# Kernel tuning notes

Measured on AMD Instinct MI355X. Metric: run time of the kernel, lower is better.

The kernel has to match this reference:

```python
import jax, jax.numpy as jnp
import numpy as np
import math

WH, WW = 7, 7          # window size
N = WH * WW            # tokens per window = 49
H = 12                 # num heads
C = 384                # dim
D = C // H             # head dim = 32
NW = 64                # num windows (56x56 map, 7x7 windows)
B = 32                 # image batch
BW = B * NW            # windowed batch = 2048


def _cpb_constants():
    # log-spaced continuous relative coords table, flattened to [(2*WH-1)*(2*WW-1), 2]
    rh = np.arange(-(WH - 1), WH, dtype=np.float32)
    rw = np.arange(-(WW - 1), WW, dtype=np.float32)
    t = np.stack(np.meshgrid(rh, rw, indexing='ij'), axis=-1)  # [13,13,2]
    t[..., 0] /= (WH - 1)
    t[..., 1] /= (WW - 1)
    t *= 8.0
    t = np.sign(t) * np.log2(np.abs(t) + 1.0) / np.log2(8.0)
    # relative position index [N*N]
    ch, cw = np.meshgrid(np.arange(WH), np.arange(WW), indexing='ij')
    cf = np.stack([ch.ravel(), cw.ravel()])            # [2, N]
    rel = cf[:, :, None] - cf[:, None, :]              # [2, N, N]
    rel = rel.transpose(1, 2, 0).astype(np.int64)      # [N, N, 2]
    rel[..., 0] += WH - 1
    rel[..., 1] += WW - 1
    rel[..., 0] *= 2 * WW - 1
    rpi = rel.sum(-1).reshape(-1)                      # [N*N]
    return jnp.asarray(t.reshape(-1, 2)), jnp.asarray(rpi)

_COORDS_TABLE, _RPI = _cpb_constants()


def setup_inputs() -> dict:
    key = jax.random.key(0)
    ks = jax.random.split(key, 8)
    x = jax.random.normal(ks[0], (BW, N, C), dtype=jnp.float32)
    # shifted-window style 0/-100 mask
    mask = jnp.where(jax.random.uniform(ks[1], (NW, N, N)) < 0.1, -100.0, 0.0).astype(jnp.float32)
    qkv_w = jax.random.normal(ks[2], (3 * C, C), dtype=jnp.float32) * 0.02
    q_bias = jnp.zeros((C,), dtype=jnp.float32)
    v_bias = jnp.zeros((C,), dtype=jnp.float32)
    logit_scale = jnp.full((H, 1, 1), math.log(10.0), dtype=jnp.float32)
    cpb_w1 = jax.random.normal(ks[3], (512, 2), dtype=jnp.float32) * 0.02
    cpb_b1 = jnp.zeros((512,), dtype=jnp.float32)
    cpb_w2 = jax.random.normal(ks[4], (H, 512), dtype=jnp.float32) * 0.02
    proj_w = jax.random.normal(ks[5], (C, C), dtype=jnp.float32) * 0.02
    proj_b = jnp.zeros((C,), dtype=jnp.float32)
    return {"x": x, "mask": mask, "qkv_w": qkv_w, "q_bias": q_bias, "v_bias": v_bias,
            "logit_scale": logit_scale, "cpb_w1": cpb_w1, "cpb_b1": cpb_b1,
            "cpb_w2": cpb_w2, "proj_w": proj_w, "proj_b": proj_b}


def reference(x, mask, qkv_w, q_bias, v_bias, logit_scale, cpb_w1, cpb_b1, cpb_w2, proj_w, proj_b):
    B_, n, c = x.shape
    # qkv projection; k has no bias (registered zeros buffer)
    qkv_bias = jnp.concatenate([q_bias, jnp.zeros_like(q_bias), v_bias])
    qkv = x @ qkv_w.T + qkv_bias                              # [B_, N, 3C]
    qkv = qkv.reshape(B_, n, 3, H, D).transpose(2, 0, 3, 1, 4)  # [3, B_, H, N, D]
    q, k, v = qkv[0], qkv[1], qkv[2]
    # cosine attention
    qn = q / jnp.clip(jnp.linalg.norm(q, axis=-1, keepdims=True), 1e-12)
    kn = k / jnp.clip(jnp.linalg.norm(k, axis=-1, keepdims=True), 1e-12)
    attn = jnp.einsum('bhnd,bhmd->bhnm', qn, kn)              # [B_, H, N, N]
    scale = jnp.exp(jnp.minimum(logit_scale, math.log(1.0 / 0.01)))  # [H,1,1]
    attn = attn * scale
    # continuous position bias MLP + gather
    hid = jax.nn.relu(_COORDS_TABLE @ cpb_w1.T + cpb_b1)      # [169, 512]
    bias_tab = hid @ cpb_w2.T                                  # [169, H]
    rpb = bias_tab[_RPI].reshape(n, n, H).transpose(2, 0, 1)  # [H, N, N]
    rpb = 16.0 * jax.nn.sigmoid(rpb)
    attn = attn + rpb[None]
    # shifted-window mask add
    nW = mask.shape[0]
    attn = attn.reshape(B_ // nW, nW, H, n, n) + mask[None, :, None]
    attn = jax.nn.softmax(attn.reshape(B_, H, n, n), axis=-1)
    out = jnp.einsum('bhnm,bhmd->bnhd', attn, v).reshape(B_, n, c)
    return out @ proj_w.T + proj_b
```

## Files before the change

### kernel.cpp

```cpp
#include <hip/hip_runtime.h>
#include <hip/hip_bf16.h>
#include <math.h>

#define NTOK 49
#define NH 12
#define HD 32
#define CDIM 384
#define NWIN 64
#define BWIN 2048

typedef __bf16 bf16x8 __attribute__((ext_vector_type(8)));
typedef __bf16 bf16x4 __attribute__((ext_vector_type(4)));
typedef float f32x4 __attribute__((ext_vector_type(4)));

__device__ __forceinline__ void gload_lds16(const void* g, void* l) {
    __builtin_amdgcn_global_load_lds((const __attribute__((address_space(1))) void*)g,
                                     (__attribute__((address_space(3))) void*)l, 16, 0, 0);
}

__global__ void cvt_f32_bf16(const float* __restrict__ src, __bf16* __restrict__ dst, int n8) {
    int i = blockIdx.x * blockDim.x + threadIdx.x;
    if (i >= n8) return;
    f32x4 a = *(const f32x4*)(src + (size_t)i * 8);
    f32x4 b = *(const f32x4*)(src + (size_t)i * 8 + 4);
    bf16x8 o;
#pragma unroll
    for (int e = 0; e < 4; ++e) { o[e] = (__bf16)a[e]; o[e + 4] = (__bf16)b[e]; }
    *(bf16x8*)(dst + (size_t)i * 8) = o;
}

__global__ void cpb_mlp_kernel(const float* __restrict__ w1, const float* __restrict__ b1,
                               const float* __restrict__ w2, float* __restrict__ bias_tab) {
    int t = blockIdx.x * blockDim.x + threadIdx.x;
    if (t >= 169 * NH) return;
    int r = t / NH, h = t - (t / NH) * NH;
    int i = r / 13, j = r - (r / 13) * 13;
    float a0 = (float)(i - 6) * (8.0f / 6.0f);
    float a1 = (float)(j - 6) * (8.0f / 6.0f);
    float c0 = copysignf(log2f(fabsf(a0) + 1.0f) * (1.0f / 3.0f), a0);
    float c1 = copysignf(log2f(fabsf(a1) + 1.0f) * (1.0f / 3.0f), a1);
    float sum = 0.f;
    for (int k = 0; k < 512; ++k) {
        float hid = c0 * w1[2 * k] + c1 * w1[2 * k + 1] + b1[k];
        hid = fmaxf(hid, 0.f);
        sum += hid * w2[h * 512 + k];
    }
    bias_tab[r * NH + h] = sum;
}

__global__ void rpbT_kernel(const float* __restrict__ bias_tab, float* __restrict__ rpbT) {
    int idx = blockIdx.x * blockDim.x + threadIdx.x;
    if (idx >= NH * NTOK * NTOK) return;
    int h = idx / (NTOK * NTOK);
    int rem = idx - h * (NTOK * NTOK);
    int kj = rem / NTOK, qi = rem - (rem / NTOK) * NTOK;
    int chi = qi / 7, cwi = qi - chi * 7;
    int chj = kj / 7, cwj = kj - chj * 7;
    int rpi = (chi - chj + 6) * 13 + (cwi - cwj + 6);
    float x = bias_tab[rpi * NH + h];
    rpbT[idx] = 16.f / (1.f + __expf(-x));
}

__global__ void maskT_kernel(const float* __restrict__ mask, float* __restrict__ maskT) {
    int idx = blockIdx.x * blockDim.x + threadIdx.x;
    if (idx >= NWIN * NTOK * NTOK) return;
    int w = idx / (NTOK * NTOK);
    int rem = idx - w * (NTOK * NTOK);
    int kj = rem / NTOK, qi = rem - (rem / NTOK) * NTOK;
    maskT[idx] = mask[(w * NTOK + qi) * NTOK + kj];
}

template <int MODE, int NBY>
__global__ __launch_bounds__(256) void gemm3(
    const __bf16* __restrict__ A, const __bf16* __restrict__ Bw,
    const float* __restrict__ qbias, const float* __restrict__ vbias,
    __bf16* __restrict__ qkvout,
    float* __restrict__ fout, const float* __restrict__ fbias)
{
    __shared__ __bf16 As[2][128 * 32];
    __shared__ __bf16 Bs[2][128 * 32];
    const int tid = threadIdx.x;
    const int chunk = (784 * NBY) >> 3;
    const int wg = (blockIdx.x & 7) * chunk + (blockIdx.x >> 3);
    const int gx = wg / NBY, gy = wg - (wg / NBY) * NBY;
    const int lane = tid & 63;
    const int wid = tid >> 6;
    const int wr = (wid >> 1) * 64;
    const int wc = (wid & 1) * 64;
    const int fr = lane & 15;
    const int fq = lane >> 4;

    f32x4 acc[4][4];
#pragma unroll
    for (int m = 0; m < 4; ++m)
#pragma unroll
        for (int n = 0; n < 4; ++n)
            acc[m][n] = (f32x4){0.f, 0.f, 0.f, 0.f};

    const int srow0 = tid >> 2, scp0 = tid & 3;
    const int srow1 = (256 + tid) >> 2, scp1 = tid & 3;
    const size_t ar0 = (size_t)(gx * 128 + srow0) * CDIM + (scp0 ^ ((srow0 >> 1) & 3)) * 8;
    const size_t ar1 = (size_t)(gx * 128 + srow1) * CDIM + (scp1 ^ ((srow1 >> 1) & 3)) * 8;
    const size_t br0 = (size_t)(gy * 128 + srow0) * CDIM + (scp0 ^ ((srow0 >> 1) & 3)) * 8;
    const size_t br1 = (size_t)(gy * 128 + srow1) * CDIM + (scp1 ^ ((srow1 >> 1) & 3)) * 8;
    const int ls0 = tid * 16, ls1 = (256 + tid) * 16;

    gload_lds16(A + ar0, (char*)&As[0][0] + ls0);
    gload_lds16(A + ar1, (char*)&As[0][0] + ls1);
    gload_lds16(Bw + br0, (char*)&Bs[0][0] + ls0);
    gload_lds16(Bw + br1, (char*)&Bs[0][0] + ls1);
    __syncthreads();

#pragma unroll
    for (int t = 0; t < 12; ++t) {
        const int cur = t & 1;
        if (t < 11) {
            const int k = (t + 1) * 32;
            gload_lds16(A + ar0 + k, (char*)&As[cur ^ 1][0] + ls0);
            gload_lds16(A + ar1 + k, (char*)&As[cur ^ 1][0] + ls1);
            gload_lds16(Bw + br0 + k, (char*)&Bs[cur ^ 1][0] + ls0);
            gload_lds16(Bw + br1 + k, (char*)&Bs[cur ^ 1][0] + ls1);
        }
        bf16x8 af[4], bfr[4];
#pragma unroll
        for (int m = 0; m < 4; ++m) {
            const int row = wr + m * 16 + fr;
            af[m] = *(const bf16x8*)&As[cur][row * 32 + (fq ^ ((row >> 1) & 3)) * 8];
        }
#pragma unroll
        for (int n = 0; n < 4; ++n) {
            const int row = wc + n * 16 + fr;
            bfr[n] = *(const bf16x8*)&Bs[cur][row * 32 + (fq ^ ((row >> 1) & 3)) * 8];
        }
#pragma unroll
        for (int m = 0; m < 4; ++m)
#pragma unroll
            for (int n = 0; n < 4; ++n)
                acc[m][n] = __builtin_amdgcn_mfma_f32_16x16x32_bf16(af[m], bfr[n], acc[m][n], 0, 0, 0);
        __syncthreads();
    }

    if (MODE == 0) {
        const int colbase = gy * 128;
        const int part = colbase / CDIM;
        const int pcolbase = colbase - part * CDIM;
        __bf16* dst = qkvout + (size_t)part * ((size_t)BWIN * NH * NTOK * HD);
#pragma unroll
        for (int m = 0; m < 4; ++m) {
#pragma unroll
            for (int r = 0; r < 4; ++r) {
                const int row = gx * 128 + wr + m * 16 + fq * 4 + r;
                const int b = row / NTOK;
                const int nn = row - b * NTOK;
#pragma unroll
                for (int n = 0; n < 4; ++n) {
                    const int pcol = pcolbase + wc + n * 16 + fr;
                    float val = acc[m][n][r];
                    if (part == 0) val += qbias[pcol];
                    if (part == 2) val += vbias[pcol];
                    const int h = pcol >> 5, d = pcol & 31;
                    dst[(((size_t)b * NH + h) * NTOK + nn) * HD + d] = (__bf16)val;
                }
            }
        }
    } else {
#pragma unroll
        for (int m = 0; m < 4; ++m) {
#pragma unroll
            for (int r = 0; r < 4; ++r) {
                const int row = gx * 128 + wr + m * 16 + fq * 4 + r;
                float* orow = fout + (size_t)row * CDIM + gy * 128 + wc;
#pragma unroll
                for (int n = 0; n < 4; ++n) {
                    const int col = gy * 128 + wc + n * 16 + fr;
                    orow[n * 16 + fr] = acc[m][n][r] + fbias[col];
                }
            }
        }
    }
}

#define WREG 15872
__global__ __launch_bounds__(256) void attn2(
    const __bf16* __restrict__ qb, const __bf16* __restrict__ kb,
    const __bf16* __restrict__ vb, const float* __restrict__ maskT,
    const float* __restrict__ rpbT, const float* __restrict__ lscale,
    __bf16* __restrict__ aout)
{
    __shared__ char smem[4 * WREG];
    const int tid = threadIdx.x;
    const int wid = tid >> 6, lane = tid & 63;
    const int bh = blockIdx.x * 4 + wid;
    const int b = bh / NH, h = bh - b * NH;
    const int w = b & (NWIN - 1);
    const int c = lane & 15, g = lane >> 4;

    char* base = smem + wid * WREG;
    __bf16* Kl = (__bf16*)base;
    __bf16* Ql = (__bf16*)(base + 5120);
    __bf16* Vl = (__bf16*)(base + 10240);
    float* invq = (float*)(base + 15360);
    float* invk = (float*)(base + 15616);
    __bf16* Pl = (__bf16*)base;

    const float sc = __expf(fminf(lscale[h], 4.6051702f));

    {
        const int row = lane;
        const size_t rb = (size_t)bh * (NTOK * HD) + (size_t)row * HD;
        bf16x8 z;
#pragma unroll
        for (int e = 0; e < 8; ++e) z[e] = (__bf16)0.f;
        {
            bf16x8 t[4];
            float ss = 0.f;
            if (row < NTOK) {
#pragma unroll
                for (int ch = 0; ch < 4; ++ch) {
                    t[ch] = *(const bf16x8*)(qb + rb + ch * 8);
#pragma unroll
                    for (int e = 0; e < 8; ++e) { float f = (float)t[ch][e]; ss += f * f; }
                }
            } else {
#pragma unroll
                for (int ch = 0; ch < 4; ++ch) t[ch] = z;
            }
#pragma unroll
            for (int ch = 0; ch < 4; ++ch) *(bf16x8*)&Ql[row * 40 + ch * 8] = t[ch];
            invq[row] = sc / fmaxf(sqrtf(ss), 1e-12f);
        }
        {
            bf16x8 t[4];
            float ss = 0.f;
            if (row < NTOK) {
#pragma unroll
                for (int ch = 0; ch < 4; ++ch) {
                    t[ch] = *(const bf16x8*)(kb + rb + ch * 8);
#pragma unroll
                    for (int e = 0; e < 8; ++e) { float f = (float)t[ch][e]; ss += f * f; }
                }
            } else {
#pragma unroll
                for (int ch = 0; ch < 4; ++ch) t[ch] = z;
            }
#pragma unroll
            for (int ch = 0; ch < 4; ++ch) *(bf16x8*)&Kl[row * 40 + ch * 8] = t[ch];
            invk[row] = 1.f / fmaxf(sqrtf(ss), 1e-12f);
        }
        {
            bf16x8 t[4];
            if (row < NTOK) {
#pragma unroll
                for (int ch = 0; ch < 4; ++ch) t[ch] = *(const bf16x8*)(vb + rb + ch * 8);
            } else {
#pragma unroll
                for (int ch = 0; ch < 4; ++ch) t[ch] = z;
            }
#pragma unroll
            for (int ch = 0; ch < 4; ++ch) *(bf16x8*)&Vl[row * 40 + ch * 8] = t[ch];
        }
    }

    bf16x8 kfr[4], qfr[4];
#pragma unroll
    for (int mt = 0; mt < 4; ++mt) kfr[mt] = *(const bf16x8*)&Kl[(mt * 16 + c) * 40 + g * 8];
#pragma unroll
    for (int nt = 0; nt < 4; ++nt) qfr[nt] = *(const bf16x8*)&Ql[(nt * 16 + c) * 40 + g * 8];
    f32x4 S[4][4];
#pragma unroll
    for (int mt = 0; mt < 4; ++mt)
#pragma unroll
        for (int nt = 0; nt < 4; ++nt) {
            S[mt][nt] = (f32x4){0.f, 0.f, 0.f, 0.f};
            S[mt][nt] = __builtin_amdgcn_mfma_f32_16x16x32_bf16(kfr[mt], qfr[nt], S[mt][nt], 0, 0, 0);
        }

    const float* rp = rpbT + h * (NTOK * NTOK);
    const float* mk = maskT + w * (NTOK * NTOK);
    float ivq[4];
#pragma unroll
    for (int nt = 0; nt < 4; ++nt) ivq[nt] = invq[nt * 16 + c];
#pragma unroll
    for (int mt = 0; mt < 4; ++mt) {
#pragma unroll
        for (int r = 0; r < 4; ++r) {
            const int k = mt * 16 + g * 4 + r;
            const float ivk = invk[k];
#pragma unroll
            for (int nt = 0; nt < 4; ++nt) {
                const int q = nt * 16 + c;
                float v = S[mt][nt][r] * ivk * ivq[nt];
                if (k < NTOK) {
                    if (q < NTOK) v += rp[k * NTOK + q] + mk[k * NTOK + q];
                } else {
                    v = -1e30f;
                }
                S[mt][nt][r] = v;
            }
        }
    }

    float rs[4];
#pragma unroll
    for (int nt = 0; nt < 4; ++nt) {
        float m = -1e30f;
#pragma unroll
        for (int mt = 0; mt < 4; ++mt)
#pragma unroll
            for (int r = 0; r < 4; ++r) m = fmaxf(m, S[mt][nt][r]);
        m = fmaxf(m, __shfl_xor(m, 16));
        m = fmaxf(m, __shfl_xor(m, 32));
        float s = 0.f;
#pragma unroll
        for (int mt = 0; mt < 4; ++mt)
#pragma unroll
            for (int r = 0; r < 4; ++r) {
                float e = __expf(S[mt][nt][r] - m);
                S[mt][nt][r] = e;
                s += e;
            }
        s += __shfl_xor(s, 16);
        s += __shfl_xor(s, 32);
        rs[nt] = 1.f / s;
    }

#pragma unroll
    for (int mt = 0; mt < 4; ++mt)
#pragma unroll
        for (int nt = 0; nt < 4; ++nt) {
            bf16x4 pk;
#pragma unroll
            for (int r = 0; r < 4; ++r) pk[r] = (__bf16)(S[mt][nt][r] * rs[nt]);
            *(bf16x4*)((char*)Pl + (nt * 16 + c) * 144 + (mt * 16 + g * 4) * 2) = pk;
        }

    bf16x8 vfr[2][2];
#pragma unroll
    for (int kt = 0; kt < 2; ++kt)
#pragma unroll
        for (int dt = 0; dt < 2; ++dt) {
            bf16x8 t;
#pragma unroll
            for (int e = 0; e < 8; ++e) t[e] = Vl[(kt * 32 + g * 8 + e) * 40 + dt * 16 + c];
            vfr[kt][dt] = t;
        }
    f32x4 O[4][2];
#pragma unroll
    for (int mt = 0; mt < 4; ++mt)
#pragma unroll
        for (int dt = 0; dt < 2; ++dt) O[mt][dt] = (f32x4){0.f, 0.f, 0.f, 0.f};
#pragma unroll
    for (int mt = 0; mt < 4; ++mt)
#pragma unroll
        for (int kt = 0; kt < 2; ++kt) {
            bf16x8 pfr = *(const bf16x8*)((char*)Pl + (mt * 16 + c) * 144 + kt * 64 + g * 16);
#pragma unroll
            for (int dt = 0; dt < 2; ++dt)
                O[mt][dt] = __builtin_amdgcn_mfma_f32_16x16x32_bf16(pfr, vfr[kt][dt], O[mt][dt], 0, 0, 0);
        }

#pragma unroll
    for (int mt = 0; mt < 4; ++mt)
#pragma unroll
        for (int r = 0; r < 4; ++r) {
            const int q = mt * 16 + g * 4 + r;
            if (q < NTOK) {
                const size_t off = ((size_t)b * NTOK + q) * CDIM + h * HD;
                aout[off + c] = (__bf16)O[mt][0][r];
                aout[off + 16 + c] = (__bf16)O[mt][1][r];
            }
        }
}

extern "C" void kernel_launch(void* const* d_in, const int* in_sizes, int n_in,
                              void* d_out, int out_size, void* d_ws, size_t ws_size,
                              hipStream_t stream) {
    const float* x      = (const float*)d_in[0];
    const float* mask   = (const float*)d_in[1];
    const float* qkv_w  = (const float*)d_in[2];
    const float* q_bias = (const float*)d_in[3];
    const float* v_bias = (const float*)d_in[4];
    const float* lscale = (const float*)d_in[5];
    const float* cpb_w1 = (const float*)d_in[6];
    const float* cpb_b1 = (const float*)d_in[7];
    const float* cpb_w2 = (const float*)d_in[8];
    const float* proj_w = (const float*)d_in[9];
    const float* proj_b = (const float*)d_in[10];
    float* out = (float*)d_out;

    const size_t QKVELEMS = (size_t)BWIN * NH * NTOK * HD;
    __bf16* qkvbuf  = (__bf16*)d_ws;
    __bf16* xbf     = qkvbuf + 3 * QKVELEMS;
    __bf16* aoutbuf = xbf;
    __bf16* qkv_wb  = xbf + QKVELEMS;
    __bf16* proj_wb = qkv_wb + 1152 * CDIM;
    float*  bias_tab = (float*)(proj_wb + CDIM * CDIM);
    float*  rpbT   = bias_tab + 169 * NH;
    float*  maskT  = rpbT + NH * NTOK * NTOK;

    hipLaunchKernelGGL(cvt_f32_bf16, dim3((int)((QKVELEMS / 8 + 255) / 256)), dim3(256), 0, stream,
                       x, xbf, (int)(QKVELEMS / 8));
    hipLaunchKernelGGL(cvt_f32_bf16, dim3((1152 * CDIM / 8 + 255) / 256), dim3(256), 0, stream,
                       qkv_w, qkv_wb, 1152 * CDIM / 8);
    hipLaunchKernelGGL(cvt_f32_bf16, dim3((CDIM * CDIM / 8 + 255) / 256), dim3(256), 0, stream,
                       proj_w, proj_wb, CDIM * CDIM / 8);
    hipLaunchKernelGGL(cpb_mlp_kernel, dim3(8), dim3(256), 0, stream,
                       cpb_w1, cpb_b1, cpb_w2, bias_tab);
    hipLaunchKernelGGL(rpbT_kernel, dim3((NH * NTOK * NTOK + 255) / 256), dim3(256), 0, stream,
                       bias_tab, rpbT);
    hipLaunchKernelGGL(maskT_kernel, dim3((NWIN * NTOK * NTOK + 255) / 256), dim3(256), 0, stream,
                       mask, maskT);
    hipLaunchKernelGGL((gemm3<0, 9>), dim3(784 * 9), dim3(256), 0, stream,
                       xbf, qkv_wb, q_bias, v_bias, qkvbuf, (float*)nullptr,
                       (const float*)nullptr);
    hipLaunchKernelGGL(attn2, dim3(BWIN * NH / 4), dim3(256), 0, stream,
                       qkvbuf, qkvbuf + QKVELEMS, qkvbuf + 2 * QKVELEMS, maskT, rpbT, lscale,
                       aoutbuf);
    hipLaunchKernelGGL((gemm3<1, 3>), dim3(784 * 3), dim3(256), 0, stream,
                       aoutbuf, proj_wb, (const float*)nullptr, (const float*)nullptr,
                       (__bf16*)nullptr, out, proj_b);
}
```

Baseline: 467.0 us.

## Triple-buffer GEMM K-loop with one barrier per step and vmcnt waits

Deepens the GEMM shared-memory pipeline from two stages to three, keeping two tile loads in flight. Each K step now uses one explicit vmcnt wait plus a single barrier instead of a full __syncthreads at the end of every iteration. The aim is to hide global-to-LDS load latency and cut synchronisation stalls in both the QKV and projection GEMMs. In exchange, LDS use rises from 32KB to 48KB per block, which may lower occupancy, and correctness now depends on the hand-written waitcnt counts.

```diff
diff --git a/kernel.cpp b/kernel.cpp
--- a/kernel.cpp
+++ b/kernel.cpp
@@ -71,14 +71,14 @@
 }
 
 template <int MODE, int NBY>
-__global__ __launch_bounds__(256) void gemm3(
+__global__ __launch_bounds__(256) void gemm4(
     const __bf16* __restrict__ A, const __bf16* __restrict__ Bw,
     const float* __restrict__ qbias, const float* __restrict__ vbias,
     __bf16* __restrict__ qkvout,
     float* __restrict__ fout, const float* __restrict__ fbias)
 {
-    __shared__ __bf16 As[2][128 * 32];
-    __shared__ __bf16 Bs[2][128 * 32];
+    __shared__ __bf16 As[3][128 * 32];
+    __shared__ __bf16 Bs[3][128 * 32];
     const int tid = threadIdx.x;
     const int chunk = (784 * NBY) >> 3;
     const int wg = (blockIdx.x & 7) * chunk + (blockIdx.x >> 3);
@@ -105,22 +105,24 @@
     const size_t br1 = (size_t)(gy * 128 + srow1) * CDIM + (scp1 ^ ((srow1 >> 1) & 3)) * 8;
     const int ls0 = tid * 16, ls1 = (256 + tid) * 16;
 
-    gload_lds16(A + ar0, (char*)&As[0][0] + ls0);
-    gload_lds16(A + ar1, (char*)&As[0][0] + ls1);
-    gload_lds16(Bw + br0, (char*)&Bs[0][0] + ls0);
-    gload_lds16(Bw + br1, (char*)&Bs[0][0] + ls1);
-    __syncthreads();
+#define STAGE4(ti, buf) do {                                            \
+        const int kk_ = (ti) * 32;                                      \
+        gload_lds16(A + ar0 + kk_, (char*)&As[buf][0] + ls0);           \
+        gload_lds16(A + ar1 + kk_, (char*)&As[buf][0] + ls1);           \
+        gload_lds16(Bw + br0 + kk_, (char*)&Bs[buf][0] + ls0);          \
+        gload_lds16(Bw + br1 + kk_, (char*)&Bs[buf][0] + ls1);          \
+    } while (0)
+
+    STAGE4(0, 0);
+    STAGE4(1, 1);
 
 #pragma unroll
     for (int t = 0; t < 12; ++t) {
-        const int cur = t & 1;
-        if (t < 11) {
-            const int k = (t + 1) * 32;
-            gload_lds16(A + ar0 + k, (char*)&As[cur ^ 1][0] + ls0);
-            gload_lds16(A + ar1 + k, (char*)&As[cur ^ 1][0] + ls1);
-            gload_lds16(Bw + br0 + k, (char*)&Bs[cur ^ 1][0] + ls0);
-            gload_lds16(Bw + br1 + k, (char*)&Bs[cur ^ 1][0] + ls1);
-        }
+        if (t < 11) asm volatile("s_waitcnt vmcnt(4)" ::: "memory");
+        else        asm volatile("s_waitcnt vmcnt(0)" ::: "memory");
+        __builtin_amdgcn_s_barrier();
+        if (t + 2 < 12) STAGE4(t + 2, (t + 2) % 3);
+        const int cur = t % 3;
         bf16x8 af[4], bfr[4];
 #pragma unroll
         for (int m = 0; m < 4; ++m) {
@@ -137,8 +139,8 @@
 #pragma unroll
             for (int n = 0; n < 4; ++n)
                 acc[m][n] = __builtin_amdgcn_mfma_f32_16x16x32_bf16(af[m], bfr[n], acc[m][n], 0, 0, 0);
-        __syncthreads();
-    }
+    }
+#undef STAGE4
 
     if (MODE == 0) {
         const int colbase = gy * 128;
@@ -410,13 +412,13 @@
                        bias_tab, rpbT);
     hipLaunchKernelGGL(maskT_kernel, dim3((NWIN * NTOK * NTOK + 255) / 256), dim3(256), 0, stream,
                        mask, maskT);
-    hipLaunchKernelGGL((gemm3<0, 9>), dim3(784 * 9), dim3(256), 0, stream,
+    hipLaunchKernelGGL((gemm4<0, 9>), dim3(784 * 9), dim3(256), 0, stream,
                        xbf, qkv_wb, q_bias, v_bias, qkvbuf, (float*)nullptr,
                        (const float*)nullptr);
     hipLaunchKernelGGL(attn2, dim3(BWIN * NH / 4), dim3(256), 0, stream,
                        qkvbuf, qkvbuf + QKVELEMS, qkvbuf + 2 * QKVELEMS, maskT, rpbT, lscale,
                        aoutbuf);
-    hipLaunchKernelGGL((gemm3<1, 3>), dim3(784 * 3), dim3(256), 0, stream,
+    hipLaunchKernelGGL((gemm4<1, 3>), dim3(784 * 3), dim3(256), 0, stream,
                        aoutbuf, proj_wb, (const float*)nullptr, (const float*)nullptr,
                        (__bf16*)nullptr, out, proj_b);
 }
```

New measurement: 462.4 us. About the same (-1.0%).

## Fuse QKV GEMM, windowed attention and projection into one per-window kernel

Applied to the files above, without the earlier changes.

Replaces the separate x conversion, QKV GEMM, attention and projection kernels with a single kernel that handles one window per block. x is converted to bf16 directly into LDS, QKV for each head is computed into LDS, attention runs per wave, and the concatenated output is projected from LDS with weights streamed from global into registers. This removes the HBM round trips for the bf16 x copy, the QKV tensor and the attention output, plus several launches. In exchange it uses about 158 KB of LDS at one block per CU, and each block re-reads the full weight matrices from cache with no LDS staging of weights.

```diff
diff --git a/kernel.cpp b/kernel.cpp
--- a/kernel.cpp
+++ b/kernel.cpp
@@ -12,11 +12,6 @@
 typedef __bf16 bf16x8 __attribute__((ext_vector_type(8)));
 typedef __bf16 bf16x4 __attribute__((ext_vector_type(4)));
 typedef float f32x4 __attribute__((ext_vector_type(4)));
-
-__device__ __forceinline__ void gload_lds16(const void* g, void* l) {
-    __builtin_amdgcn_global_load_lds((const __attribute__((address_space(1))) void*)g,
-                                     (__attribute__((address_space(3))) void*)l, 16, 0, 0);
-}
 
 __global__ void cvt_f32_bf16(const float* __restrict__ src, __bf16* __restrict__ dst, int n8) {
     int i = blockIdx.x * blockDim.x + threadIdx.x;
@@ -70,306 +65,332 @@
     maskT[idx] = mask[(w * NTOK + qi) * NTOK + kj];
 }
 
-template <int MODE, int NBY>
-__global__ __launch_bounds__(256) void gemm3(
-    const __bf16* __restrict__ A, const __bf16* __restrict__ Bw,
+#define SWZ(row, byteInRow) ((row) * 768 + ((byteInRow) ^ (((row) & 7) << 4)))
+
+__global__ __launch_bounds__(256, 1) void fused_win(
+    const float* __restrict__ x, const __bf16* __restrict__ Wqkv,
+    const __bf16* __restrict__ Wproj,
     const float* __restrict__ qbias, const float* __restrict__ vbias,
-    __bf16* __restrict__ qkvout,
-    float* __restrict__ fout, const float* __restrict__ fbias)
+    const float* __restrict__ maskT, const float* __restrict__ rpbT,
+    const float* __restrict__ lscale, const float* __restrict__ projb,
+    float* __restrict__ out)
 {
-    __shared__ __bf16 As[2][128 * 32];
-    __shared__ __bf16 Bs[2][128 * 32];
-    const int tid = threadIdx.x;
-    const int chunk = (784 * NBY) >> 3;
-    const int wg = (blockIdx.x & 7) * chunk + (blockIdx.x >> 3);
-    const int gx = wg / NBY, gy = wg - (wg / NBY) * NBY;
-    const int lane = tid & 63;
-    const int wid = tid >> 6;
-    const int wr = (wid >> 1) * 64;
-    const int wc = (wid & 1) * 64;
-    const int fr = lane & 15;
-    const int fq = lane >> 4;
-
-    f32x4 acc[4][4];
-#pragma unroll
-    for (int m = 0; m < 4; ++m)
-#pragma unroll
-        for (int n = 0; n < 4; ++n)
-            acc[m][n] = (f32x4){0.f, 0.f, 0.f, 0.f};
-
-    const int srow0 = tid >> 2, scp0 = tid & 3;
-    const int srow1 = (256 + tid) >> 2, scp1 = tid & 3;
-    const size_t ar0 = (size_t)(gx * 128 + srow0) * CDIM + (scp0 ^ ((srow0 >> 1) & 3)) * 8;
-    const size_t ar1 = (size_t)(gx * 128 + srow1) * CDIM + (scp1 ^ ((srow1 >> 1) & 3)) * 8;
-    const size_t br0 = (size_t)(gy * 128 + srow0) * CDIM + (scp0 ^ ((srow0 >> 1) & 3)) * 8;
-    const size_t br1 = (size_t)(gy * 128 + srow1) * CDIM + (scp1 ^ ((srow1 >> 1) & 3)) * 8;
-    const int ls0 = tid * 16, ls1 = (256 + tid) * 16;
-
-    gload_lds16(A + ar0, (char*)&As[0][0] + ls0);
-    gload_lds16(A + ar1, (char*)&As[0][0] + ls1);
-    gload_lds16(Bw + br0, (char*)&Bs[0][0] + ls0);
-    gload_lds16(Bw + br1, (char*)&Bs[0][0] + ls1);
-    __syncthreads();
-
-#pragma unroll
-    for (int t = 0; t < 12; ++t) {
-        const int cur = t & 1;
-        if (t < 11) {
-            const int k = (t + 1) * 32;
-            gload_lds16(A + ar0 + k, (char*)&As[cur ^ 1][0] + ls0);
-            gload_lds16(A + ar1 + k, (char*)&As[cur ^ 1][0] + ls1);
-            gload_lds16(Bw + br0 + k, (char*)&Bs[cur ^ 1][0] + ls0);
-            gload_lds16(Bw + br1 + k, (char*)&Bs[cur ^ 1][0] + ls1);
-        }
-        bf16x8 af[4], bfr[4];
-#pragma unroll
-        for (int m = 0; m < 4; ++m) {
-            const int row = wr + m * 16 + fr;
-            af[m] = *(const bf16x8*)&As[cur][row * 32 + (fq ^ ((row >> 1) & 3)) * 8];
-        }
-#pragma unroll
-        for (int n = 0; n < 4; ++n) {
-            const int row = wc + n * 16 + fr;
-            bfr[n] = *(const bf16x8*)&Bs[cur][row * 32 + (fq ^ ((row >> 1) & 3)) * 8];
-        }
-#pragma unroll
-        for (int m = 0; m < 4; ++m)
-#pragma unroll
-            for (int n = 0; n < 4; ++n)
-                acc[m][n] = __builtin_amdgcn_mfma_f32_16x16x32_bf16(af[m], bfr[n], acc[m][n], 0, 0, 0);
-        __syncthreads();
-    }
-
-    if (MODE == 0) {
-        const int colbase = gy * 128;
-        const int part = colbase / CDIM;
-        const int pcolbase = colbase - part * CDIM;
-        __bf16* dst = qkvout + (size_t)part * ((size_t)BWIN * NH * NTOK * HD);
-#pragma unroll
-        for (int m = 0; m < 4; ++m) {
-#pragma unroll
-            for (int r = 0; r < 4; ++r) {
-                const int row = gx * 128 + wr + m * 16 + fq * 4 + r;
-                const int b = row / NTOK;
-                const int nn = row - b * NTOK;
-#pragma unroll
-                for (int n = 0; n < 4; ++n) {
-                    const int pcol = pcolbase + wc + n * 16 + fr;
-                    float val = acc[m][n][r];
-                    if (part == 0) val += qbias[pcol];
-                    if (part == 2) val += vbias[pcol];
-                    const int h = pcol >> 5, d = pcol & 31;
-                    dst[(((size_t)b * NH + h) * NTOK + nn) * HD + d] = (__bf16)val;
-                }
-            }
-        }
-    } else {
-#pragma unroll
-        for (int m = 0; m < 4; ++m) {
-#pragma unroll
-            for (int r = 0; r < 4; ++r) {
-                const int row = gx * 128 + wr + m * 16 + fq * 4 + r;
-                float* orow = fout + (size_t)row * CDIM + gy * 128 + wc;
-#pragma unroll
-                for (int n = 0; n < 4; ++n) {
-                    const int col = gy * 128 + wc + n * 16 + fr;
-                    orow[n * 16 + fr] = acc[m][n][r] + fbias[col];
-                }
-            }
-        }
-    }
-}
-
-#define WREG 15872
-__global__ __launch_bounds__(256) void attn2(
-    const __bf16* __restrict__ qb, const __bf16* __restrict__ kb,
-    const __bf16* __restrict__ vb, const float* __restrict__ maskT,
-    const float* __restrict__ rpbT, const float* __restrict__ lscale,
-    __bf16* __restrict__ aout)
-{
-    __shared__ char smem[4 * WREG];
+    __shared__ char smem[161792];
+    char* XW = smem;
+    char* AT = smem + 49152;
+    char* AO = smem + 112640;
+
     const int tid = threadIdx.x;
     const int wid = tid >> 6, lane = tid & 63;
-    const int bh = blockIdx.x * 4 + wid;
-    const int b = bh / NH, h = bh - b * NH;
-    const int w = b & (NWIN - 1);
     const int c = lane & 15, g = lane >> 4;
-
-    char* base = smem + wid * WREG;
+    const int blk = blockIdx.x;
+    const int w = blk & (NWIN - 1);
+
+#pragma unroll
+    for (int i = 0; i < 12; ++i) {
+        const int s = i * 256 + tid;
+        const int row = s / 48, cp = s - (s / 48) * 48;
+        bf16x8 v;
+        if (row < NTOK) {
+            const float* p = x + ((size_t)blk * NTOK + row) * CDIM + cp * 8;
+            f32x4 a = *(const f32x4*)p;
+            f32x4 b = *(const f32x4*)(p + 4);
+#pragma unroll
+            for (int e = 0; e < 4; ++e) { v[e] = (__bf16)a[e]; v[e + 4] = (__bf16)b[e]; }
+        } else {
+#pragma unroll
+            for (int e = 0; e < 8; ++e) v[e] = (__bf16)0.f;
+        }
+        *(bf16x8*)(XW + SWZ(row, cp * 16)) = v;
+    }
+    __syncthreads();
+
+    char* base = AT + wid * 15872;
     __bf16* Kl = (__bf16*)base;
     __bf16* Ql = (__bf16*)(base + 5120);
     __bf16* Vl = (__bf16*)(base + 10240);
     float* invq = (float*)(base + 15360);
     float* invk = (float*)(base + 15616);
-    __bf16* Pl = (__bf16*)base;
-
-    const float sc = __expf(fminf(lscale[h], 4.6051702f));
+    char* Pl = base;
+
+    for (int hi = 0; hi < 3; ++hi) {
+        const int h = hi * 4 + wid;
+        const float sc = __expf(fminf(lscale[h], 4.6051702f));
+
+        f32x4 acc[4][6];
+#pragma unroll
+        for (int m = 0; m < 4; ++m)
+#pragma unroll
+            for (int n = 0; n < 6; ++n) acc[m][n] = (f32x4){0.f, 0.f, 0.f, 0.f};
+
+        size_t boff[6];
+#pragma unroll
+        for (int n = 0; n < 6; ++n)
+            boff[n] = (size_t)((n >> 1) * CDIM + 32 * h + (n & 1) * 16 + c) * CDIM + g * 8;
+
+#define QLD(arr, t) do {                                              \
+        arr[0] = *(const bf16x8*)(Wqkv + boff[0] + (t) * 32);         \
+        arr[1] = *(const bf16x8*)(Wqkv + boff[1] + (t) * 32);         \
+        arr[2] = *(const bf16x8*)(Wqkv + boff[2] + (t) * 32);         \
+        arr[3] = *(const bf16x8*)(Wqkv + boff[3] + (t) * 32);         \
+        arr[4] = *(const bf16x8*)(Wqkv + boff[4] + (t) * 32);         \
+        arr[5] = *(const bf16x8*)(Wqkv + boff[5] + (t) * 32);         \
+    } while (0)
+
+        bf16x8 b0[6], b1[6], b2[6];
+        QLD(b0, 0); QLD(b1, 1); QLD(b2, 2);
+
+#pragma unroll
+        for (int t = 0; t < 12; ++t) {
+            bf16x8 af[4];
+#pragma unroll
+            for (int m = 0; m < 4; ++m)
+                af[m] = *(const bf16x8*)(XW + SWZ(m * 16 + c, t * 64 + g * 16));
+            if (t % 3 == 0) {
+#pragma unroll
+                for (int m = 0; m < 4; ++m)
+#pragma unroll
+                    for (int n = 0; n < 6; ++n)
+                        acc[m][n] = __builtin_amdgcn_mfma_f32_16x16x32_bf16(af[m], b0[n], acc[m][n], 0, 0, 0);
+                if (t + 3 < 12) QLD(b0, t + 3);
+            } else if (t % 3 == 1) {
+#pragma unroll
+                for (int m = 0; m < 4; ++m)
+#pragma unroll
+                    for (int n = 0; n < 6; ++n)
+                        acc[m][n] = __builtin_amdgcn_mfma_f32_16x16x32_bf16(af[m], b1[n], acc[m][n], 0, 0, 0);
+                if (t + 3 < 12) QLD(b1, t + 3);
+            } else {
+#pragma unroll
+                for (int m = 0; m < 4; ++m)
+#pragma unroll
+                    for (int n = 0; n < 6; ++n)
+                        acc[m][n] = __builtin_amdgcn_mfma_f32_16x16x32_bf16(af[m], b2[n], acc[m][n], 0, 0, 0);
+                if (t + 3 < 12) QLD(b2, t + 3);
+            }
+        }
+#undef QLD
+
+        float qb_[2], vb_[2];
+#pragma unroll
+        for (int n2 = 0; n2 < 2; ++n2) {
+            qb_[n2] = qbias[32 * h + n2 * 16 + c];
+            vb_[n2] = vbias[32 * h + n2 * 16 + c];
+        }
+#pragma unroll
+        for (int m = 0; m < 4; ++m)
+#pragma unroll
+            for (int n = 0; n < 6; ++n) {
+                __bf16* dst = (n < 2) ? Ql : (n < 4 ? Kl : Vl);
+                const float bias = (n < 2) ? qb_[n & 1] : (n >= 4 ? vb_[n & 1] : 0.f);
+                const int col = (n & 1) * 16 + c;
+#pragma unroll
+                for (int r = 0; r < 4; ++r) {
+                    const int row = m * 16 + g * 4 + r;
+                    dst[row * 40 + col] = (__bf16)(acc[m][n][r] + bias);
+                }
+            }
+
+        {
+            const int row = lane;
+            float ss = 0.f;
+#pragma unroll
+            for (int ch = 0; ch < 4; ++ch) {
+                bf16x8 tq = *(const bf16x8*)&Ql[row * 40 + ch * 8];
+#pragma unroll
+                for (int e = 0; e < 8; ++e) { float f = (float)tq[e]; ss += f * f; }
+            }
+            invq[row] = sc / fmaxf(sqrtf(ss), 1e-12f);
+            ss = 0.f;
+#pragma unroll
+            for (int ch = 0; ch < 4; ++ch) {
+                bf16x8 tk = *(const bf16x8*)&Kl[row * 40 + ch * 8];
+#pragma unroll
+                for (int e = 0; e < 8; ++e) { float f = (float)tk[e]; ss += f * f; }
+            }
+            invk[row] = 1.f / fmaxf(sqrtf(ss), 1e-12f);
+        }
+
+        bf16x8 kfr[4], qfr[4];
+#pragma unroll
+        for (int mt = 0; mt < 4; ++mt) kfr[mt] = *(const bf16x8*)&Kl[(mt * 16 + c) * 40 + g * 8];
+#pragma unroll
+        for (int nt = 0; nt < 4; ++nt) qfr[nt] = *(const bf16x8*)&Ql[(nt * 16 + c) * 40 + g * 8];
+        f32x4 S[4][4];
+#pragma unroll
+        for (int mt = 0; mt < 4; ++mt)
+#pragma unroll
+            for (int nt = 0; nt < 4; ++nt) {
+                S[mt][nt] = (f32x4){0.f, 0.f, 0.f, 0.f};
+                S[mt][nt] = __builtin_amdgcn_mfma_f32_16x16x32_bf16(kfr[mt], qfr[nt], S[mt][nt], 0, 0, 0);
+            }
+
+        const float* rp = rpbT + h * (NTOK * NTOK);
+        const float* mk = maskT + w * (NTOK * NTOK);
+        float ivq[4];
+#pragma unroll
+        for (int nt = 0; nt < 4; ++nt) ivq[nt] = invq[nt * 16 + c];
+#pragma unroll
+        for (int mt = 0; mt < 4; ++mt) {
+#pragma unroll
+            for (int r = 0; r < 4; ++r) {
+                const int k = mt * 16 + g * 4 + r;
+                const float ivk = invk[k];
+#pragma unroll
+                for (int nt = 0; nt < 4; ++nt) {
+                    const int q = nt * 16 + c;
+                    float v = S[mt][nt][r] * ivk * ivq[nt];
+                    if (k < NTOK) {
+                        if (q < NTOK) v += rp[k * NTOK + q] + mk[k * NTOK + q];
+                    } else {
+                        v = -1e30f;
+                    }
+                    S[mt][nt][r] = v;
+                }
+            }
+        }
+
+        float rs[4];
+#pragma unroll
+        for (int nt = 0; nt < 4; ++nt) {
+            float m = -1e30f;
+#pragma unroll
+            for (int mt = 0; mt < 4; ++mt)
+#pragma unroll
+                for (int r = 0; r < 4; ++r) m = fmaxf(m, S[mt][nt][r]);
+            m = fmaxf(m, __shfl_xor(m, 16));
+            m = fmaxf(m, __shfl_xor(m, 32));
+            float s = 0.f;
+#pragma unroll
+            for (int mt = 0; mt < 4; ++mt)
+#pragma unroll
+                for (int r = 0; r < 4; ++r) {
+                    float e = __expf(S[mt][nt][r] - m);
+                    S[mt][nt][r] = e;
+                    s += e;
+                }
+            s += __shfl_xor(s, 16);
+            s += __shfl_xor(s, 32);
+            rs[nt] = 1.f / s;
+        }
+
+#pragma unroll
+        for (int mt = 0; mt < 4; ++mt)
+#pragma unroll
+            for (int nt = 0; nt < 4; ++nt) {
+                bf16x4 pk;
+#pragma unroll
+                for (int r = 0; r < 4; ++r) pk[r] = (__bf16)(S[mt][nt][r] * rs[nt]);
+                *(bf16x4*)(Pl + (nt * 16 + c) * 144 + (mt * 16 + g * 4) * 2) = pk;
+            }
+
+        bf16x8 vfr[2][2];
+#pragma unroll
+        for (int kt = 0; kt < 2; ++kt)
+#pragma unroll
+            for (int dt = 0; dt < 2; ++dt) {
+                bf16x8 t;
+#pragma unroll
+                for (int e = 0; e < 8; ++e) t[e] = Vl[(kt * 32 + g * 8 + e) * 40 + dt * 16 + c];
+                vfr[kt][dt] = t;
+            }
+        f32x4 O[4][2];
+#pragma unroll
+        for (int mt = 0; mt < 4; ++mt)
+#pragma unroll
+            for (int dt = 0; dt < 2; ++dt) O[mt][dt] = (f32x4){0.f, 0.f, 0.f, 0.f};
+#pragma unroll
+        for (int mt = 0; mt < 4; ++mt)
+#pragma unroll
+            for (int kt = 0; kt < 2; ++kt) {
+                bf16x8 pfr = *(const bf16x8*)(Pl + (mt * 16 + c) * 144 + kt * 64 + g * 16);
+#pragma unroll
+                for (int dt = 0; dt < 2; ++dt)
+                    O[mt][dt] = __builtin_amdgcn_mfma_f32_16x16x32_bf16(pfr, vfr[kt][dt], O[mt][dt], 0, 0, 0);
+            }
+
+#pragma unroll
+        for (int mt = 0; mt < 4; ++mt)
+#pragma unroll
+            for (int r = 0; r < 4; ++r) {
+                const int q = mt * 16 + g * 4 + r;
+                *(__bf16*)(AO + SWZ(q, (32 * h + c) * 2)) = (__bf16)O[mt][0][r];
+                *(__bf16*)(AO + SWZ(q, (32 * h + 16 + c) * 2)) = (__bf16)O[mt][1][r];
+            }
+    }
+
+    __syncthreads();
 
     {
-        const int row = lane;
-        const size_t rb = (size_t)bh * (NTOK * HD) + (size_t)row * HD;
-        bf16x8 z;
-#pragma unroll
-        for (int e = 0; e < 8; ++e) z[e] = (__bf16)0.f;
-        {
-            bf16x8 t[4];
-            float ss = 0.f;
-            if (row < NTOK) {
-#pragma unroll
-                for (int ch = 0; ch < 4; ++ch) {
-                    t[ch] = *(const bf16x8*)(qb + rb + ch * 8);
-#pragma unroll
-                    for (int e = 0; e < 8; ++e) { float f = (float)t[ch][e]; ss += f * f; }
+        f32x4 acc[4][6];
+#pragma unroll
+        for (int m = 0; m < 4; ++m)
+#pragma unroll
+            for (int n = 0; n < 6; ++n) acc[m][n] = (f32x4){0.f, 0.f, 0.f, 0.f};
+
+        size_t boff[6];
+#pragma unroll
+        for (int n = 0; n < 6; ++n)
+            boff[n] = (size_t)(wid * 96 + n * 16 + c) * CDIM + g * 8;
+
+#define PLD(arr, t) do {                                               \
+        arr[0] = *(const bf16x8*)(Wproj + boff[0] + (t) * 32);         \
+        arr[1] = *(const bf16x8*)(Wproj + boff[1] + (t) * 32);         \
+        arr[2] = *(const bf16x8*)(Wproj + boff[2] + (t) * 32);         \
+        arr[3] = *(const bf16x8*)(Wproj + boff[3] + (t) * 32);         \
+        arr[4] = *(const bf16x8*)(Wproj + boff[4] + (t) * 32);         \
+        arr[5] = *(const bf16x8*)(Wproj + boff[5] + (t) * 32);         \
+    } while (0)
+
+        bf16x8 b0[6], b1[6], b2[6];
+        PLD(b0, 0); PLD(b1, 1); PLD(b2, 2);
+
+#pragma unroll
+        for (int t = 0; t < 12; ++t) {
+            bf16x8 af[4];
+#pragma unroll
+            for (int m = 0; m < 4; ++m)
+                af[m] = *(const bf16x8*)(AO + SWZ(m * 16 + c, t * 64 + g * 16));
+            if (t % 3 == 0) {
+#pragma unroll
+                for (int m = 0; m < 4; ++m)
+#pragma unroll
+                    for (int n = 0; n < 6; ++n)
+                        acc[m][n] = __builtin_amdgcn_mfma_f32_16x16x32_bf16(af[m], b0[n], acc[m][n], 0, 0, 0);
+                if (t + 3 < 12) PLD(b0, t + 3);
+            } else if (t % 3 == 1) {
+#pragma unroll
+                for (int m = 0; m < 4; ++m)
+#pragma unroll
+                    for (int n = 0; n < 6; ++n)
+                        acc[m][n] = __builtin_amdgcn_mfma_f32_16x16x32_bf16(af[m], b1[n], acc[m][n], 0, 0, 0);
+                if (t + 3 < 12) PLD(b1, t + 3);
+            } else {
+#pragma unroll
+                for (int m = 0; m < 4; ++m)
+#pragma unroll
+                    for (int n = 0; n < 6; ++n)
+                        acc[m][n] = __builtin_amdgcn_mfma_f32_16x16x32_bf16(af[m], b2[n], acc[m][n], 0, 0, 0);
+                if (t + 3 < 12) PLD(b2, t + 3);
+            }
+        }
+#undef PLD
+
+        float pb[6];
+#pragma unroll
+        for (int n = 0; n < 6; ++n) pb[n] = projb[wid * 96 + n * 16 + c];
+#pragma unroll
+        for (int m = 0; m < 4; ++m)
+#pragma unroll
+            for (int r = 0; r < 4; ++r) {
+                const int trow = m * 16 + g * 4 + r;
+                if (trow < NTOK) {
+                    float* orow = out + ((size_t)blk * NTOK + trow) * CDIM + wid * 96;
+#pragma unroll
+                    for (int n = 0; n < 6; ++n) orow[n * 16 + c] = acc[m][n][r] + pb[n];
                 }
-            } else {
-#pragma unroll
-                for (int ch = 0; ch < 4; ++ch) t[ch] = z;
-            }
-#pragma unroll
-            for (int ch = 0; ch < 4; ++ch) *(bf16x8*)&Ql[row * 40 + ch * 8] = t[ch];
-            invq[row] = sc / fmaxf(sqrtf(ss), 1e-12f);
-        }
-        {
-            bf16x8 t[4];
-            float ss = 0.f;
-            if (row < NTOK) {
-#pragma unroll
-                for (int ch = 0; ch < 4; ++ch) {
-                    t[ch] = *(const bf16x8*)(kb + rb + ch * 8);
-#pragma unroll
-                    for (int e = 0; e < 8; ++e) { float f = (float)t[ch][e]; ss += f * f; }
-                }
-            } else {
-#pragma unroll
-                for (int ch = 0; ch < 4; ++ch) t[ch] = z;
-            }
-#pragma unroll
-            for (int ch = 0; ch < 4; ++ch) *(bf16x8*)&Kl[row * 40 + ch * 8] = t[ch];
-            invk[row] = 1.f / fmaxf(sqrtf(ss), 1e-12f);
-        }
-        {
-            bf16x8 t[4];
-            if (row < NTOK) {
-#pragma unroll
-                for (int ch = 0; ch < 4; ++ch) t[ch] = *(const bf16x8*)(vb + rb + ch * 8);
-            } else {
-#pragma unroll
-                for (int ch = 0; ch < 4; ++ch) t[ch] = z;
-            }
-#pragma unroll
-            for (int ch = 0; ch < 4; ++ch) *(bf16x8*)&Vl[row * 40 + ch * 8] = t[ch];
-        }
+            }
     }
-
-    bf16x8 kfr[4], qfr[4];
-#pragma unroll
-    for (int mt = 0; mt < 4; ++mt) kfr[mt] = *(const bf16x8*)&Kl[(mt * 16 + c) * 40 + g * 8];
-#pragma unroll
-    for (int nt = 0; nt < 4; ++nt) qfr[nt] = *(const bf16x8*)&Ql[(nt * 16 + c) * 40 + g * 8];
-    f32x4 S[4][4];
-#pragma unroll
-    for (int mt = 0; mt < 4; ++mt)
-#pragma unroll
-        for (int nt = 0; nt < 4; ++nt) {
-            S[mt][nt] = (f32x4){0.f, 0.f, 0.f, 0.f};
-            S[mt][nt] = __builtin_amdgcn_mfma_f32_16x16x32_bf16(kfr[mt], qfr[nt], S[mt][nt], 0, 0, 0);
-        }
-
-    const float* rp = rpbT + h * (NTOK * NTOK);
-    const float* mk = maskT + w * (NTOK * NTOK);
-    float ivq[4];
-#pragma unroll
-    for (int nt = 0; nt < 4; ++nt) ivq[nt] = invq[nt * 16 + c];
-#pragma unroll
-    for (int mt = 0; mt < 4; ++mt) {
-#pragma unroll
-        for (int r = 0; r < 4; ++r) {
-            const int k = mt * 16 + g * 4 + r;
-            const float ivk = invk[k];
-#pragma unroll
-            for (int nt = 0; nt < 4; ++nt) {
-                const int q = nt * 16 + c;
-                float v = S[mt][nt][r] * ivk * ivq[nt];
-                if (k < NTOK) {
-                    if (q < NTOK) v += rp[k * NTOK + q] + mk[k * NTOK + q];
-                } else {
-                    v = -1e30f;
-                }
-                S[mt][nt][r] = v;
-            }
-        }
-    }
-
-    float rs[4];
-#pragma unroll
-    for (int nt = 0; nt < 4; ++nt) {
-        float m = -1e30f;
-#pragma unroll
-        for (int mt = 0; mt < 4; ++mt)
-#pragma unroll
-            for (int r = 0; r < 4; ++r) m = fmaxf(m, S[mt][nt][r]);
-        m = fmaxf(m, __shfl_xor(m, 16));
-        m = fmaxf(m, __shfl_xor(m, 32));
-        float s = 0.f;
-#pragma unroll
-        for (int mt = 0; mt < 4; ++mt)
-#pragma unroll
-            for (int r = 0; r < 4; ++r) {
-                float e = __expf(S[mt][nt][r] - m);
-                S[mt][nt][r] = e;
-                s += e;
-            }
-        s += __shfl_xor(s, 16);
-        s += __shfl_xor(s, 32);
-        rs[nt] = 1.f / s;
-    }
-
-#pragma unroll
-    for (int mt = 0; mt < 4; ++mt)
-#pragma unroll
-        for (int nt = 0; nt < 4; ++nt) {
-            bf16x4 pk;
-#pragma unroll
-            for (int r = 0; r < 4; ++r) pk[r] = (__bf16)(S[mt][nt][r] * rs[nt]);
-            *(bf16x4*)((char*)Pl + (nt * 16 + c) * 144 + (mt * 16 + g * 4) * 2) = pk;
-        }
-
-    bf16x8 vfr[2][2];
-#pragma unroll
-    for (int kt = 0; kt < 2; ++kt)
-#pragma unroll
-        for (int dt = 0; dt < 2; ++dt) {
-            bf16x8 t;
-#pragma unroll
-            for (int e = 0; e < 8; ++e) t[e] = Vl[(kt * 32 + g * 8 + e) * 40 + dt * 16 + c];
-            vfr[kt][dt] = t;
-        }
-    f32x4 O[4][2];
-#pragma unroll
-    for (int mt = 0; mt < 4; ++mt)
-#pragma unroll
-        for (int dt = 0; dt < 2; ++dt) O[mt][dt] = (f32x4){0.f, 0.f, 0.f, 0.f};
-#pragma unroll
-    for (int mt = 0; mt < 4; ++mt)
-#pragma unroll
-        for (int kt = 0; kt < 2; ++kt) {
-            bf16x8 pfr = *(const bf16x8*)((char*)Pl + (mt * 16 + c) * 144 + kt * 64 + g * 16);
-#pragma unroll
-            for (int dt = 0; dt < 2; ++dt)
-                O[mt][dt] = __builtin_amdgcn_mfma_f32_16x16x32_bf16(pfr, vfr[kt][dt], O[mt][dt], 0, 0, 0);
-        }
-
-#pragma unroll
-    for (int mt = 0; mt < 4; ++mt)
-#pragma unroll
-        for (int r = 0; r < 4; ++r) {
-            const int q = mt * 16 + g * 4 + r;
-            if (q < NTOK) {
-                const size_t off = ((size_t)b * NTOK + q) * CDIM + h * HD;
-                aout[off + c] = (__bf16)O[mt][0][r];
-                aout[off + 16 + c] = (__bf16)O[mt][1][r];
-            }
-        }
 }
 
 extern "C" void kernel_launch(void* const* d_in, const int* in_sizes, int n_in,
@@ -388,18 +409,12 @@
     const float* proj_b = (const float*)d_in[10];
     float* out = (float*)d_out;
 
-    const size_t QKVELEMS = (size_t)BWIN * NH * NTOK * HD;
-    __bf16* qkvbuf  = (__bf16*)d_ws;
-    __bf16* xbf     = qkvbuf + 3 * QKVELEMS;
-    __bf16* aoutbuf = xbf;
-    __bf16* qkv_wb  = xbf + QKVELEMS;
+    __bf16* qkv_wb  = (__bf16*)d_ws;
     __bf16* proj_wb = qkv_wb + 1152 * CDIM;
     float*  bias_tab = (float*)(proj_wb + CDIM * CDIM);
     float*  rpbT   = bias_tab + 169 * NH;
     float*  maskT  = rpbT + NH * NTOK * NTOK;
 
-    hipLaunchKernelGGL(cvt_f32_bf16, dim3((int)((QKVELEMS / 8 + 255) / 256)), dim3(256), 0, stream,
-                       x, xbf, (int)(QKVELEMS / 8));
     hipLaunchKernelGGL(cvt_f32_bf16, dim3((1152 * CDIM / 8 + 255) / 256), dim3(256), 0, stream,
                        qkv_w, qkv_wb, 1152 * CDIM / 8);
     hipLaunchKernelGGL(cvt_f32_bf16, dim3((CDIM * CDIM / 8 + 255) / 256), dim3(256), 0, stream,
@@ -410,13 +425,6 @@
                        bias_tab, rpbT);
     hipLaunchKernelGGL(maskT_kernel, dim3((NWIN * NTOK * NTOK + 255) / 256), dim3(256), 0, stream,
                        mask, maskT);
-    hipLaunchKernelGGL((gemm3<0, 9>), dim3(784 * 9), dim3(256), 0, stream,
-                       xbf, qkv_wb, q_bias, v_bias, qkvbuf, (float*)nullptr,
-                       (const float*)nullptr);
-    hipLaunchKernelGGL(attn2, dim3(BWIN * NH / 4), dim3(256), 0, stream,
-                       qkvbuf, qkvbuf + QKVELEMS, qkvbuf + 2 * QKVELEMS, maskT, rpbT, lscale,
-                       aoutbuf);
-    hipLaunchKernelGGL((gemm3<1, 3>), dim3(784 * 3), dim3(256), 0, stream,
-                       aoutbuf, proj_wb, (const float*)nullptr, (const float*)nullptr,
-                       (__bf16*)nullptr, out, proj_b);
-}
+    hipLaunchKernelGGL(fused_win, dim3(BWIN), dim3(256), 0, stream,
+                       x, qkv_wb, proj_wb, q_bias, v_bias, maskT, rpbT, lscale, proj_b, out);
+}
```

New measurement: 554.8 us. +18.8%, slower.
